# Optimization experiments

Hardware: AMD Instinct MI355X
Metric: run time of the kernel (lower is better)

Reference implementation:

```python
import jax, jax.numpy as jnp
import numpy as np

B, N, C = 8, 4096, 64          # graphs, points per graph, feature dim
RATIO = 0.25
M = int(N * RATIO)             # 1024 sampled centroids per graph
R = 0.2                        # radius (points live in the unit cube)
K = 64                         # max_num_neighbors in the forward
BIG = 1e10


def fps_single(pos):
    """Farthest point sampling on one cloud. pos: [N,3] -> [M] local indices.
    Deterministic start at index 0 (PyG uses a random start; math is identical)."""
    n = pos.shape[0]

    def step(carry, _):
        mind, last = carry
        d = jnp.sum((pos - pos[last]) ** 2, axis=-1)      # [N]
        mind = jnp.minimum(mind, d)
        nxt = jnp.argmax(mind)
        return (mind, nxt), nxt

    init = (jnp.full((n,), BIG, pos.dtype), jnp.int32(0))
    _, rest = jax.lax.scan(step, init, None, length=M - 1)
    return jnp.concatenate([jnp.zeros((1,), rest.dtype), rest])


def setup_inputs() -> dict:
    key = jax.random.key(0)
    ks = jax.random.split(key, 8)
    x = jax.random.normal(ks[0], (B * N, C), dtype=jnp.float32)
    pos = jax.random.uniform(ks[1], (B * N, 3), dtype=jnp.float32)
    batch = jnp.repeat(jnp.arange(B, dtype=jnp.int64), N)
    seed_idx = jnp.arange(B * N, dtype=jnp.int64)
    d_in, h, f_out = C + 3, 128, 256
    W1 = jax.random.normal(ks[2], (d_in, h), dtype=jnp.float32) / np.sqrt(d_in)
    b1 = jnp.zeros((h,), jnp.float32)
    W2 = jax.random.normal(ks[3], (h, h), dtype=jnp.float32) / np.sqrt(h)
    b2 = jnp.zeros((h,), jnp.float32)
    W3 = jax.random.normal(ks[4], (h, f_out), dtype=jnp.float32) / np.sqrt(h)
    b3 = jnp.zeros((f_out,), jnp.float32)
    return {"x": x, "pos": pos, "batch": batch, "seed_idx": seed_idx,
            "W1": W1, "b1": b1, "W2": W2, "b2": b2, "W3": W3, "b3": b3}


def reference(x, pos, batch, seed_idx, W1, b1, W2, b2, W3, b3):
    posb = pos.reshape(B, N, 3)
    xb = x.reshape(B, N, C)

    # --- FPS per graph (batch is block-contiguous with N points per graph) ---
    idx_local = jax.vmap(fps_single)(posb)                     # [B, M]
    ctr = jax.vmap(lambda p, i: p[i])(posb, idx_local)         # [B, M, 3]

    # --- radius neighbor search: up to K neighbors within r of each centroid ---
    d2 = jnp.sum((ctr[:, :, None, :] - posb[:, None, :, :]) ** 2, axis=-1)  # [B,M,N]
    d2m = jnp.where(d2 < R * R, d2, BIG)
    neg_d, nbr = jax.lax.top_k(-d2m, K)                        # K nearest within r
    valid = (-neg_d) < R * R                                   # [B, M, K]

    # --- PointConv: msg = MLP([x_j, pos_j - pos_i]), max-aggregate ---
    x_j = jax.vmap(lambda a, i: a[i])(xb, nbr)                 # [B, M, K, C]
    pos_j = jax.vmap(lambda p, i: p[i])(posb, nbr)             # [B, M, K, 3]
    msg = jnp.concatenate([x_j, pos_j - ctr[:, :, None, :]], axis=-1)  # [B,M,K,C+3]
    h = jax.nn.relu(msg @ W1 + b1)
    h = jax.nn.relu(h @ W2 + b2)
    h = jax.nn.relu(h @ W3 + b3)                               # [B, M, K, 256]
    h = jnp.where(valid[..., None], h, -BIG)
    out = jnp.max(h, axis=2)                                   # [B, M, 256]
    out = jnp.where(jnp.any(valid, axis=-1)[..., None], out, 0.0)

    # --- gather sampled outputs back to the flat layout ---
    idx_flat = (idx_local + jnp.arange(B)[:, None] * N).reshape(-1)  # [B*M]
    x_out = out.reshape(B * M, -1)
    pos_out = pos[idx_flat]
    batch_out = batch[idx_flat]
    seed_out = seed_idx[idx_flat]
    return x_out, pos_out, batch_out, seed_out
```

## Files before the change

### kernel.cpp

```cpp
#include <hip/hip_runtime.h>
#include <stdint.h>

#define BB 8
#define NN 4096
#define CC 64
#define MM 1024
#define EE (BB*MM)
#define KK 64
#define F3 256
#define SM 104
#define SH 136
#define CAP 768

typedef __bf16 bf16x8 __attribute__((ext_vector_type(8)));
typedef float floatx4 __attribute__((ext_vector_type(4)));

#define DPP_MAXSTEP(ctrl, rmask) { \
    unsigned o = (unsigned)__builtin_amdgcn_update_dpp(0, (int)v, ctrl, rmask, 0xf, false); \
    v = v > o ? v : o; }
__device__ __forceinline__ unsigned wave_umax_u32(unsigned v) {
  DPP_MAXSTEP(0x111, 0xf)
  DPP_MAXSTEP(0x112, 0xf)
  DPP_MAXSTEP(0x114, 0xf)
  DPP_MAXSTEP(0x118, 0xf)
  DPP_MAXSTEP(0x142, 0xa)
  DPP_MAXSTEP(0x143, 0xc)
  return (unsigned)__builtin_amdgcn_readlane((int)v, 63);
}
#define DPP_MINSTEP(ctrl, rmask) { \
    unsigned o = (unsigned)__builtin_amdgcn_update_dpp((int)0xffffffffu, (int)v, ctrl, rmask, 0xf, false); \
    v = v < o ? v : o; }
__device__ __forceinline__ unsigned wave_umin_u32(unsigned v) {
  DPP_MINSTEP(0x111, 0xf)
  DPP_MINSTEP(0x112, 0xf)
  DPP_MINSTEP(0x114, 0xf)
  DPP_MINSTEP(0x118, 0xf)
  DPP_MINSTEP(0x142, 0xa)
  DPP_MINSTEP(0x143, 0xc)
  return (unsigned)__builtin_amdgcn_readlane((int)v, 63);
}

__global__ __launch_bounds__(256) void fps_prep_kernel(
    const float* __restrict__ pos,
    const float* __restrict__ W1, const float* __restrict__ W2, const float* __restrict__ W3,
    int* __restrict__ fpsIdx, float* __restrict__ ctr,
    __bf16* __restrict__ W1t, __bf16* __restrict__ W2t, __bf16* __restrict__ W3t,
    float4* __restrict__ pos4) {
  __shared__ float4 sP4[NN];
  __shared__ unsigned long long sRed[2][4];
  const int blk = blockIdx.x;
  const int t = threadIdx.x;

  if (blk >= BB) {
    if (blk < 248) {
      const int i0 = (blk - 8) * 256 + t;
      if (i0 < 128 * 96) {
        const int n = i0 / 96, k = i0 % 96;
        W1t[i0] = (k < 67) ? (__bf16)W1[k * 128 + n] : (__bf16)0.0f;
      } else if (i0 < 128 * 96 + 128 * 128) {
        const int i = i0 - 128 * 96;
        const int n = i / 128, k = i % 128;
        W2t[i] = (__bf16)W2[k * 128 + n];
      } else {
        const int i = i0 - (128 * 96 + 128 * 128);
        const int n = i / 128, k = i % 128;
        W3t[i] = (__bf16)W3[k * 256 + n];
      }
    } else {
      const int i = (blk - 248) * 256 + t;
      pos4[i] = make_float4(pos[(long)i * 3 + 0], pos[(long)i * 3 + 1],
                            pos[(long)i * 3 + 2], 0.0f);
    }
    return;
  }

  const int g = blk;
  const int lane = t & 63, wv = t >> 6;
  float px[16], py[16], pz[16], mind[16];
#pragma unroll
  for (int j = 0; j < 16; ++j) {
    const int p = t + (j << 8);
    const long base = ((long)g * NN + p) * 3;
    px[j] = pos[base + 0];
    py[j] = pos[base + 1];
    pz[j] = pos[base + 2];
    mind[j] = 1e10f;
    sP4[p] = make_float4(px[j], py[j], pz[j], 0.0f);
  }
  __syncthreads();
  float wx = sP4[0].x, wy = sP4[0].y, wz = sP4[0].z;
  int win0 = 0, win1 = 0, win2 = 0, win3 = 0;
  for (int s = 1; s < MM; ++s) {
    unsigned bb = 0u, bidx = (unsigned)t;
#pragma unroll
    for (int j = 0; j < 16; ++j) {
      const float dx = __fsub_rn(px[j], wx);
      const float dy = __fsub_rn(py[j], wy);
      const float dz = __fsub_rn(pz[j], wz);
      const float d2 = __fadd_rn(__fadd_rn(__fmul_rn(dx, dx), __fmul_rn(dy, dy)), __fmul_rn(dz, dz));
      mind[j] = fminf(mind[j], d2);
      const unsigned mb = __float_as_uint(mind[j]);
      if (mb > bb) { bb = mb; bidx = (unsigned)(t + (j << 8)); }
    }
    const unsigned maxv = wave_umax_u32(bb);
    const unsigned cand = (bb == maxv) ? bidx : 0xffffffffu;
    const unsigned widx_w = wave_umin_u32(cand);
    if (lane == 0)
      sRed[s & 1][wv] = ((unsigned long long)maxv << 32) | (unsigned long long)(~widx_w);
    __syncthreads();
    unsigned long long m = sRed[s & 1][0];
#pragma unroll
    for (int w = 1; w < 4; ++w) {
      const unsigned long long o = sRed[s & 1][w];
      m = o > m ? o : m;
    }
    const int widx = (int)(~(unsigned)m);
    const float4 wp = sP4[widx];
    wx = wp.x; wy = wp.y; wz = wp.z;
    win0 = (s == t)       ? widx : win0;
    win1 = (s == t + 256) ? widx : win1;
    win2 = (s == t + 512) ? widx : win2;
    win3 = (s == t + 768) ? widx : win3;
  }
  {
    const long e0 = (long)g * MM + t;
    const float4 p0 = sP4[win0];
    fpsIdx[e0] = win0;
    ctr[e0 * 3 + 0] = p0.x; ctr[e0 * 3 + 1] = p0.y; ctr[e0 * 3 + 2] = p0.z;
    const long e1 = e0 + 256;
    const float4 p1 = sP4[win1];
    fpsIdx[e1] = win1;
    ctr[e1 * 3 + 0] = p1.x; ctr[e1 * 3 + 1] = p1.y; ctr[e1 * 3 + 2] = p1.z;
    const long e2 = e0 + 512;
    const float4 p2 = sP4[win2];
    fpsIdx[e2] = win2;
    ctr[e2 * 3 + 0] = p2.x; ctr[e2 * 3 + 1] = p2.y; ctr[e2 * 3 + 2] = p2.z;
    const long e3 = e0 + 768;
    const float4 p3 = sP4[win3];
    fpsIdx[e3] = win3;
    ctr[e3 * 3 + 0] = p3.x; ctr[e3 * 3 + 1] = p3.y; ctr[e3 * 3 + 2] = p3.z;
  }
}

__global__ __launch_bounds__(512) void mlp_kernel(const float* __restrict__ x,
    const float4* __restrict__ pos4, const float* __restrict__ ctr,
    const int* __restrict__ fpsIdx,
    const __bf16* __restrict__ W1t, const __bf16* __restrict__ W2t,
    const __bf16* __restrict__ W3t,
    const float* __restrict__ b1, const float* __restrict__ b2,
    const float* __restrict__ b3,
    float* __restrict__ outX, float* __restrict__ outP,
    float* __restrict__ outB, float* __restrict__ outS) {
  __shared__ __align__(16) __bf16 sMsg[64 * SM];
  __shared__ __align__(16) __bf16 sH[64 * SH];
  __shared__ int sSel[KK];
  __shared__ int sCnt;
  unsigned long long* sDI = (unsigned long long*)sMsg;

  const int e = blockIdx.x;
  const int t = threadIdx.x;
  const int b = e >> 10;
  const int lane = t & 63, wv = t >> 6;

  if (t == 0) sCnt = 0;
  const float cx = ctr[(long)e * 3 + 0];
  const float cy = ctr[(long)e * 3 + 1];
  const float cz = ctr[(long)e * 3 + 2];
  if (t < 3) outP[(long)e * 3 + t] = ctr[(long)e * 3 + t];
  if (t == 3) { outB[e] = (float)b; outS[e] = (float)(b * NN + fpsIdx[e]); }
  const float R2 = (float)(0.2 * 0.2);
  __syncthreads();

#pragma unroll
  for (int q = 0; q < NN / 512; ++q) {
    const int p = t + q * 512;
    const float4 P = pos4[b * NN + p];
    const float dx = __fsub_rn(cx, P.x);
    const float dy = __fsub_rn(cy, P.y);
    const float dz = __fsub_rn(cz, P.z);
    const float d2 = __fadd_rn(__fadd_rn(__fmul_rn(dx, dx), __fmul_rn(dy, dy)), __fmul_rn(dz, dz));
    const bool v = d2 < R2;
    const unsigned long long mask = __ballot(v);
    int wbase = 0;
    if (lane == 0 && mask) wbase = atomicAdd(&sCnt, (int)__popcll(mask));
    wbase = __shfl(wbase, 0);
    if (v) {
      const int off = wbase + (int)__popcll(mask & ((1ull << lane) - 1ull));
      if (off < CAP)
        sDI[off] = ((unsigned long long)__float_as_uint(d2) << 32) | (unsigned)p;
    }
  }
  __syncthreads();
  int cnt = sCnt; cnt = cnt > CAP ? CAP : cnt;
  const int nsel = cnt < KK ? cnt : KK;

  for (int i = t; i < cnt; i += 512) {
    const unsigned long long my = sDI[i];
    int rank = 0;
#pragma unroll 8
    for (int j = 0; j < cnt; ++j) rank += (sDI[j] < my) ? 1 : 0;
    if (rank < KK) sSel[rank] = (int)(unsigned)(my & 0xffffffffu);
  }
  __syncthreads();
  cnt = nsel;

  {
    const int r = t >> 3, p = t & 7;
    float4 a = make_float4(0.f, 0.f, 0.f, 0.f), c4 = a;
    if (r < cnt) {
      const float* xr = x + (long)(b * NN + sSel[r]) * CC + p * 8;
      a  = *(const float4*)xr;
      c4 = *(const float4*)(xr + 4);
    }
    __bf16 o[8] = {(__bf16)a.x, (__bf16)a.y, (__bf16)a.z, (__bf16)a.w,
                   (__bf16)c4.x, (__bf16)c4.y, (__bf16)c4.z, (__bf16)c4.w};
    *(uint4*)&sMsg[r * SM + p * 8] = *(uint4*)o;
  }
  if (t < 64) {
    const int r = t;
    __bf16 d0 = (__bf16)0.0f, d1 = (__bf16)0.0f, d2v = (__bf16)0.0f;
    if (r < cnt) {
      const float4 P = pos4[b * NN + sSel[r]];
      d0  = (__bf16)__fsub_rn(P.x, cx);
      d1  = (__bf16)__fsub_rn(P.y, cy);
      d2v = (__bf16)__fsub_rn(P.z, cz);
    }
    sMsg[r * SM + 64] = d0;
    sMsg[r * SM + 65] = d1;
    sMsg[r * SM + 66] = d2v;
    for (int c = 67; c < SM; ++c) sMsg[r * SM + c] = (__bf16)0.0f;
  }
  __syncthreads();

  const int l15 = lane & 15, quad = lane >> 4;
  {
    floatx4 acc[4] = {};
    const __bf16* wrow = W1t + (wv * 16 + l15) * 96;
#pragma unroll
    for (int ks = 0; ks < 3; ++ks) {
      const bf16x8 bfrag = *(const bf16x8*)(wrow + ks * 32 + quad * 8);
#pragma unroll
      for (int mt = 0; mt < 4; ++mt) {
        const bf16x8 afrag = *(const bf16x8*)&sMsg[(mt * 16 + l15) * SM + ks * 32 + quad * 8];
        acc[mt] = __builtin_amdgcn_mfma_f32_16x16x32_bf16(afrag, bfrag, acc[mt], 0, 0, 0);
      }
    }
    const int col = wv * 16 + l15;
    const float bias = b1[col];
#pragma unroll
    for (int mt = 0; mt < 4; ++mt)
#pragma unroll
      for (int rg = 0; rg < 4; ++rg) {
        const int row = mt * 16 + quad * 4 + rg;
        float v = acc[mt][rg] + bias;
        v = v > 0.0f ? v : 0.0f;
        sH[row * SH + col] = (__bf16)v;
      }
  }
  __syncthreads();
  {
    floatx4 acc[4] = {};
    const __bf16* wrow = W2t + (wv * 16 + l15) * 128;
#pragma unroll
    for (int ks = 0; ks < 4; ++ks) {
      const bf16x8 bfrag = *(const bf16x8*)(wrow + ks * 32 + quad * 8);
#pragma unroll
      for (int mt = 0; mt < 4; ++mt) {
        const bf16x8 afrag = *(const bf16x8*)&sH[(mt * 16 + l15) * SH + ks * 32 + quad * 8];
        acc[mt] = __builtin_amdgcn_mfma_f32_16x16x32_bf16(afrag, bfrag, acc[mt], 0, 0, 0);
      }
    }
    __syncthreads();
    const int col = wv * 16 + l15;
    const float bias = b2[col];
#pragma unroll
    for (int mt = 0; mt < 4; ++mt)
#pragma unroll
      for (int rg = 0; rg < 4; ++rg) {
        const int row = mt * 16 + quad * 4 + rg;
        float v = acc[mt][rg] + bias;
        v = v > 0.0f ? v : 0.0f;
        sH[row * SH + col] = (__bf16)v;
      }
  }
  __syncthreads();
  {
    floatx4 acc[2][4] = {};
#pragma unroll
    for (int ks = 0; ks < 4; ++ks) {
      bf16x8 afrag[4];
#pragma unroll
      for (int mt = 0; mt < 4; ++mt)
        afrag[mt] = *(const bf16x8*)&sH[(mt * 16 + l15) * SH + ks * 32 + quad * 8];
#pragma unroll
      for (int i = 0; i < 2; ++i) {
        const bf16x8 bfrag = *(const bf16x8*)(W3t + ((wv * 2 + i) * 16 + l15) * 128 + ks * 32 + quad * 8);
#pragma unroll
        for (int mt = 0; mt < 4; ++mt)
          acc[i][mt] = __builtin_amdgcn_mfma_f32_16x16x32_bf16(afrag[mt], bfrag, acc[i][mt], 0, 0, 0);
      }
    }
#pragma unroll
    for (int i = 0; i < 2; ++i) {
      const int col = (wv * 2 + i) * 16 + l15;
      const float bias = b3[col];
      float mx = 0.0f;
#pragma unroll
      for (int mt = 0; mt < 4; ++mt)
#pragma unroll
        for (int rg = 0; rg < 4; ++rg) {
          const int row = mt * 16 + quad * 4 + rg;
          float v = acc[i][mt][rg] + bias;
          v = v > 0.0f ? v : 0.0f;
          if (row < cnt) mx = fmaxf(mx, v);
        }
      mx = fmaxf(mx, __shfl_xor(mx, 16));
      mx = fmaxf(mx, __shfl_xor(mx, 32));
      if (quad == 0) outX[(long)e * F3 + col] = mx;
    }
  }
}

extern "C" void kernel_launch(void* const* d_in, const int* in_sizes, int n_in,
                              void* d_out, int out_size, void* d_ws, size_t ws_size,
                              hipStream_t stream) {
  const float* x   = (const float*)d_in[0];
  const float* pos = (const float*)d_in[1];
  const float* W1  = (const float*)d_in[4];
  const float* b1  = (const float*)d_in[5];
  const float* W2  = (const float*)d_in[6];
  const float* b2  = (const float*)d_in[7];
  const float* W3  = (const float*)d_in[8];
  const float* b3  = (const float*)d_in[9];

  char* ws = (char*)d_ws;
  int*    fpsIdx = (int*)(ws);
  float*  ctr    = (float*)(ws + 32768);
  __bf16* W1t    = (__bf16*)(ws + 131072);
  __bf16* W2t    = (__bf16*)(ws + 155648);
  __bf16* W3t    = (__bf16*)(ws + 188416);
  float4* pos4   = (float4*)(ws + 253952);

  float* outX = (float*)d_out;
  float* outP = outX + (long)EE * F3;
  float* outB = outP + (long)EE * 3;
  float* outS = outB + EE;

  fps_prep_kernel<<<376, 256, 0, stream>>>(pos, W1, W2, W3,
                                           fpsIdx, ctr, W1t, W2t, W3t, pos4);
  mlp_kernel<<<EE, 512, 0, stream>>>(x, pos4, ctr, fpsIdx, W1t, W2t, W3t,
                                     b1, b2, b3, outX, outP, outB, outS);
}
```

Baseline: 828.0 us.

## Fuse FPS and MLP into one persistent-ticket kernel with streaming progress flags

Merges the FPS/prep kernel and the per-centroid MLP kernel into one launch. Blocks take roles from an atomic ticket counter: the first eight run FPS and publish progress flags every 32 centroids, and the rest spin-wait on those flags so they can process centroids while FPS is still running. Centroid items are interleaved across graphs so the earliest ready centroids of all graphs are consumed first. The goal is to hide the serial FPS latency behind the MLP work. In exchange it adds spin-waiting, a memset launch, 64KB of shared memory per block that can lower occupancy, and it depends on the FPS blocks staying resident and running at raised priority.

```diff
diff --git a/kernel.cpp b/kernel.cpp
--- a/kernel.cpp
+++ b/kernel.cpp
@@ -40,283 +40,298 @@
   return (unsigned)__builtin_amdgcn_readlane((int)v, 63);
 }
 
-__global__ __launch_bounds__(256) void fps_prep_kernel(
-    const float* __restrict__ pos,
-    const float* __restrict__ W1, const float* __restrict__ W2, const float* __restrict__ W3,
+
+__global__ __launch_bounds__(512) void fused_kernel(
+    const float* __restrict__ x, const float* __restrict__ pos,
+    const float* __restrict__ W1, const float* __restrict__ b1,
+    const float* __restrict__ W2, const float* __restrict__ b2,
+    const float* __restrict__ W3, const float* __restrict__ b3,
     int* __restrict__ fpsIdx, float* __restrict__ ctr,
     __bf16* __restrict__ W1t, __bf16* __restrict__ W2t, __bf16* __restrict__ W3t,
-    float4* __restrict__ pos4) {
-  __shared__ float4 sP4[NN];
-  __shared__ unsigned long long sRed[2][4];
-  const int blk = blockIdx.x;
+    float4* __restrict__ pos4, unsigned* __restrict__ ctl,
+    float* __restrict__ outX, float* __restrict__ outP,
+    float* __restrict__ outB, float* __restrict__ outS) {
+  __shared__ __align__(16) unsigned char sBuf[65600];
+  __shared__ unsigned sRole;
+
   const int t = threadIdx.x;
 
-  if (blk >= BB) {
-    if (blk < 248) {
-      const int i0 = (blk - 8) * 256 + t;
-      if (i0 < 128 * 96) {
-        const int n = i0 / 96, k = i0 % 96;
-        W1t[i0] = (k < 67) ? (__bf16)W1[k * 128 + n] : (__bf16)0.0f;
-      } else if (i0 < 128 * 96 + 128 * 128) {
-        const int i = i0 - 128 * 96;
-        const int n = i / 128, k = i % 128;
-        W2t[i] = (__bf16)W2[k * 128 + n];
+  if (t == 0)
+    sRole = __hip_atomic_fetch_add(&ctl[288], 1u, __ATOMIC_RELAXED, __HIP_MEMORY_SCOPE_AGENT);
+  __syncthreads();
+  const unsigned role = sRole;
+
+  if (role < BB) {
+    const int g = (int)role;
+    float4* sP4 = (float4*)sBuf;
+    unsigned long long* sRed = (unsigned long long*)(sBuf + 65536);
+
+    for (int k = g * 11776 + t; k < (g + 1) * 11776; k += 512) {
+      if (k < 12288) {
+        const int n = k / 96, kk = k % 96;
+        W1t[k] = (kk < 67) ? (__bf16)W1[kk * 128 + n] : (__bf16)0.0f;
+      } else if (k < 28672) {
+        const int i = k - 12288, n = i / 128, kk = i % 128;
+        W2t[i] = (__bf16)W2[kk * 128 + n];
+      } else if (k < 61440) {
+        const int i = k - 28672, n = i / 128, kk = i % 128;
+        W3t[i] = (__bf16)W3[kk * 256 + n];
       } else {
-        const int i = i0 - (128 * 96 + 128 * 128);
-        const int n = i / 128, k = i % 128;
-        W3t[i] = (__bf16)W3[k * 256 + n];
-      }
-    } else {
-      const int i = (blk - 248) * 256 + t;
-      pos4[i] = make_float4(pos[(long)i * 3 + 0], pos[(long)i * 3 + 1],
-                            pos[(long)i * 3 + 2], 0.0f);
+        const int i = k - 61440;
+        pos4[i] = make_float4(pos[(long)i * 3 + 0], pos[(long)i * 3 + 1],
+                              pos[(long)i * 3 + 2], 0.0f);
+      }
+    }
+    __threadfence();
+    __syncthreads();
+    if (t == 0)
+      __hip_atomic_fetch_add(&ctl[0], 1u, __ATOMIC_RELEASE, __HIP_MEMORY_SCOPE_AGENT);
+
+    __builtin_amdgcn_s_setprio(1);
+
+    const int lane = t & 63, wv = t >> 6;
+    float px[16], py[16], pz[16], mind[16];
+    if (t < 256) {
+#pragma unroll
+      for (int j = 0; j < 16; ++j) {
+        const int p = t + (j << 8);
+        const long base = ((long)g * NN + p) * 3;
+        px[j] = pos[base + 0];
+        py[j] = pos[base + 1];
+        pz[j] = pos[base + 2];
+        mind[j] = 1e10f;
+        sP4[p] = make_float4(px[j], py[j], pz[j], 0.0f);
+      }
+    }
+    __syncthreads();
+    float wx = 0.f, wy = 0.f, wz = 0.f;
+    if (t < 256) { const float4 w0 = sP4[0]; wx = w0.x; wy = w0.y; wz = w0.z; }
+    if (t == 0) {
+      const long e0 = (long)g * MM;
+      ctr[e0 * 3 + 0] = px[0]; ctr[e0 * 3 + 1] = py[0]; ctr[e0 * 3 + 2] = pz[0];
+      fpsIdx[e0] = 0;
+    }
+    for (int s = 1; s < MM; ++s) {
+      if (t < 256) {
+        unsigned bb = 0u, bidx = (unsigned)t;
+#pragma unroll
+        for (int j = 0; j < 16; ++j) {
+          const float dx = __fsub_rn(px[j], wx);
+          const float dy = __fsub_rn(py[j], wy);
+          const float dz = __fsub_rn(pz[j], wz);
+          const float d2 = __fadd_rn(__fadd_rn(__fmul_rn(dx, dx), __fmul_rn(dy, dy)), __fmul_rn(dz, dz));
+          mind[j] = fminf(mind[j], d2);
+          const unsigned mb = __float_as_uint(mind[j]);
+          if (mb > bb) { bb = mb; bidx = (unsigned)(t + (j << 8)); }
+        }
+        const unsigned maxv = wave_umax_u32(bb);
+        const unsigned cand = (bb == maxv) ? bidx : 0xffffffffu;
+        const unsigned widx_w = wave_umin_u32(cand);
+        if (lane == 0)
+          sRed[(s & 1) * 4 + wv] = ((unsigned long long)maxv << 32) | (unsigned long long)(~widx_w);
+      }
+      __syncthreads();
+      if (t < 256) {
+        unsigned long long m = sRed[(s & 1) * 4 + 0];
+#pragma unroll
+        for (int w = 1; w < 4; ++w) {
+          const unsigned long long o = sRed[(s & 1) * 4 + w];
+          m = o > m ? o : m;
+        }
+        const int widx = (int)(~(unsigned)m);
+        const float4 wp = sP4[widx];
+        wx = wp.x; wy = wp.y; wz = wp.z;
+        if (t == 0) {
+          const long eo = (long)g * MM + s;
+          ctr[eo * 3 + 0] = wp.x; ctr[eo * 3 + 1] = wp.y; ctr[eo * 3 + 2] = wp.z;
+          fpsIdx[eo] = widx;
+          if ((s & 31) == 31)
+            __hip_atomic_store(&ctl[32 * (g + 1)], (unsigned)(s + 1),
+                               __ATOMIC_RELEASE, __HIP_MEMORY_SCOPE_AGENT);
+        }
+      }
     }
     return;
   }
 
-  const int g = blk;
-  const int lane = t & 63, wv = t >> 6;
-  float px[16], py[16], pz[16], mind[16];
-#pragma unroll
-  for (int j = 0; j < 16; ++j) {
-    const int p = t + (j << 8);
-    const long base = ((long)g * NN + p) * 3;
-    px[j] = pos[base + 0];
-    py[j] = pos[base + 1];
-    pz[j] = pos[base + 2];
-    mind[j] = 1e10f;
-    sP4[p] = make_float4(px[j], py[j], pz[j], 0.0f);
-  }
-  __syncthreads();
-  float wx = sP4[0].x, wy = sP4[0].y, wz = sP4[0].z;
-  int win0 = 0, win1 = 0, win2 = 0, win3 = 0;
-  for (int s = 1; s < MM; ++s) {
-    unsigned bb = 0u, bidx = (unsigned)t;
-#pragma unroll
-    for (int j = 0; j < 16; ++j) {
-      const float dx = __fsub_rn(px[j], wx);
-      const float dy = __fsub_rn(py[j], wy);
-      const float dz = __fsub_rn(pz[j], wz);
+  {
+    const int item = (int)role - BB;
+    if (item >= EE) return;
+    const int g = item & 7, sidx = item >> 3;
+    const int e = g * MM + sidx;
+    const int b = g;
+
+    __bf16* sMsg = (__bf16*)sBuf;
+    __bf16* sH   = (__bf16*)(sBuf + 13312);
+    int* sSel    = (int*)(sBuf + 30720);
+    int* sCnt    = (int*)(sBuf + 30976);
+    unsigned long long* sDI = (unsigned long long*)sBuf;
+
+    if (t == 0) {
+      while (__hip_atomic_load(&ctl[0], __ATOMIC_ACQUIRE, __HIP_MEMORY_SCOPE_AGENT) < (unsigned)BB)
+        __builtin_amdgcn_s_sleep(8);
+      while (__hip_atomic_load(&ctl[32 * (g + 1)], __ATOMIC_ACQUIRE, __HIP_MEMORY_SCOPE_AGENT)
+             <= (unsigned)sidx)
+        __builtin_amdgcn_s_sleep(8);
+      *sCnt = 0;
+    }
+    __syncthreads();
+
+    const int lane = t & 63, wv = t >> 6;
+    const float cx = ctr[(long)e * 3 + 0];
+    const float cy = ctr[(long)e * 3 + 1];
+    const float cz = ctr[(long)e * 3 + 2];
+    if (t < 3) outP[(long)e * 3 + t] = ctr[(long)e * 3 + t];
+    if (t == 3) { outB[e] = (float)b; outS[e] = (float)(b * NN + fpsIdx[e]); }
+    const float R2 = (float)(0.2 * 0.2);
+
+#pragma unroll
+    for (int q = 0; q < NN / 512; ++q) {
+      const int p = t + q * 512;
+      const float4 P = pos4[b * NN + p];
+      const float dx = __fsub_rn(cx, P.x);
+      const float dy = __fsub_rn(cy, P.y);
+      const float dz = __fsub_rn(cz, P.z);
       const float d2 = __fadd_rn(__fadd_rn(__fmul_rn(dx, dx), __fmul_rn(dy, dy)), __fmul_rn(dz, dz));
-      mind[j] = fminf(mind[j], d2);
-      const unsigned mb = __float_as_uint(mind[j]);
-      if (mb > bb) { bb = mb; bidx = (unsigned)(t + (j << 8)); }
-    }
-    const unsigned maxv = wave_umax_u32(bb);
-    const unsigned cand = (bb == maxv) ? bidx : 0xffffffffu;
-    const unsigned widx_w = wave_umin_u32(cand);
-    if (lane == 0)
-      sRed[s & 1][wv] = ((unsigned long long)maxv << 32) | (unsigned long long)(~widx_w);
-    __syncthreads();
-    unsigned long long m = sRed[s & 1][0];
-#pragma unroll
-    for (int w = 1; w < 4; ++w) {
-      const unsigned long long o = sRed[s & 1][w];
-      m = o > m ? o : m;
-    }
-    const int widx = (int)(~(unsigned)m);
-    const float4 wp = sP4[widx];
-    wx = wp.x; wy = wp.y; wz = wp.z;
-    win0 = (s == t)       ? widx : win0;
-    win1 = (s == t + 256) ? widx : win1;
-    win2 = (s == t + 512) ? widx : win2;
-    win3 = (s == t + 768) ? widx : win3;
-  }
-  {
-    const long e0 = (long)g * MM + t;
-    const float4 p0 = sP4[win0];
-    fpsIdx[e0] = win0;
-    ctr[e0 * 3 + 0] = p0.x; ctr[e0 * 3 + 1] = p0.y; ctr[e0 * 3 + 2] = p0.z;
-    const long e1 = e0 + 256;
-    const float4 p1 = sP4[win1];
-    fpsIdx[e1] = win1;
-    ctr[e1 * 3 + 0] = p1.x; ctr[e1 * 3 + 1] = p1.y; ctr[e1 * 3 + 2] = p1.z;
-    const long e2 = e0 + 512;
-    const float4 p2 = sP4[win2];
-    fpsIdx[e2] = win2;
-    ctr[e2 * 3 + 0] = p2.x; ctr[e2 * 3 + 1] = p2.y; ctr[e2 * 3 + 2] = p2.z;
-    const long e3 = e0 + 768;
-    const float4 p3 = sP4[win3];
-    fpsIdx[e3] = win3;
-    ctr[e3 * 3 + 0] = p3.x; ctr[e3 * 3 + 1] = p3.y; ctr[e3 * 3 + 2] = p3.z;
-  }
-}
-
-__global__ __launch_bounds__(512) void mlp_kernel(const float* __restrict__ x,
-    const float4* __restrict__ pos4, const float* __restrict__ ctr,
-    const int* __restrict__ fpsIdx,
-    const __bf16* __restrict__ W1t, const __bf16* __restrict__ W2t,
-    const __bf16* __restrict__ W3t,
-    const float* __restrict__ b1, const float* __restrict__ b2,
-    const float* __restrict__ b3,
-    float* __restrict__ outX, float* __restrict__ outP,
-    float* __restrict__ outB, float* __restrict__ outS) {
-  __shared__ __align__(16) __bf16 sMsg[64 * SM];
-  __shared__ __align__(16) __bf16 sH[64 * SH];
-  __shared__ int sSel[KK];
-  __shared__ int sCnt;
-  unsigned long long* sDI = (unsigned long long*)sMsg;
-
-  const int e = blockIdx.x;
-  const int t = threadIdx.x;
-  const int b = e >> 10;
-  const int lane = t & 63, wv = t >> 6;
-
-  if (t == 0) sCnt = 0;
-  const float cx = ctr[(long)e * 3 + 0];
-  const float cy = ctr[(long)e * 3 + 1];
-  const float cz = ctr[(long)e * 3 + 2];
-  if (t < 3) outP[(long)e * 3 + t] = ctr[(long)e * 3 + t];
-  if (t == 3) { outB[e] = (float)b; outS[e] = (float)(b * NN + fpsIdx[e]); }
-  const float R2 = (float)(0.2 * 0.2);
-  __syncthreads();
-
-#pragma unroll
-  for (int q = 0; q < NN / 512; ++q) {
-    const int p = t + q * 512;
-    const float4 P = pos4[b * NN + p];
-    const float dx = __fsub_rn(cx, P.x);
-    const float dy = __fsub_rn(cy, P.y);
-    const float dz = __fsub_rn(cz, P.z);
-    const float d2 = __fadd_rn(__fadd_rn(__fmul_rn(dx, dx), __fmul_rn(dy, dy)), __fmul_rn(dz, dz));
-    const bool v = d2 < R2;
-    const unsigned long long mask = __ballot(v);
-    int wbase = 0;
-    if (lane == 0 && mask) wbase = atomicAdd(&sCnt, (int)__popcll(mask));
-    wbase = __shfl(wbase, 0);
-    if (v) {
-      const int off = wbase + (int)__popcll(mask & ((1ull << lane) - 1ull));
-      if (off < CAP)
-        sDI[off] = ((unsigned long long)__float_as_uint(d2) << 32) | (unsigned)p;
-    }
-  }
-  __syncthreads();
-  int cnt = sCnt; cnt = cnt > CAP ? CAP : cnt;
-  const int nsel = cnt < KK ? cnt : KK;
-
-  for (int i = t; i < cnt; i += 512) {
-    const unsigned long long my = sDI[i];
-    int rank = 0;
+      const bool v = d2 < R2;
+      const unsigned long long mask = __ballot(v);
+      int wbase = 0;
+      if (lane == 0 && mask) wbase = atomicAdd(sCnt, (int)__popcll(mask));
+      wbase = __shfl(wbase, 0);
+      if (v) {
+        const int off = wbase + (int)__popcll(mask & ((1ull << lane) - 1ull));
+        if (off < CAP)
+          sDI[off] = ((unsigned long long)__float_as_uint(d2) << 32) | (unsigned)p;
+      }
+    }
+    __syncthreads();
+    int cnt = *sCnt; cnt = cnt > CAP ? CAP : cnt;
+    const int nsel = cnt < KK ? cnt : KK;
+
+    for (int i = t; i < cnt; i += 512) {
+      const unsigned long long my = sDI[i];
+      int rank = 0;
 #pragma unroll 8
-    for (int j = 0; j < cnt; ++j) rank += (sDI[j] < my) ? 1 : 0;
-    if (rank < KK) sSel[rank] = (int)(unsigned)(my & 0xffffffffu);
-  }
-  __syncthreads();
-  cnt = nsel;
-
-  {
-    const int r = t >> 3, p = t & 7;
-    float4 a = make_float4(0.f, 0.f, 0.f, 0.f), c4 = a;
-    if (r < cnt) {
-      const float* xr = x + (long)(b * NN + sSel[r]) * CC + p * 8;
-      a  = *(const float4*)xr;
-      c4 = *(const float4*)(xr + 4);
-    }
-    __bf16 o[8] = {(__bf16)a.x, (__bf16)a.y, (__bf16)a.z, (__bf16)a.w,
-                   (__bf16)c4.x, (__bf16)c4.y, (__bf16)c4.z, (__bf16)c4.w};
-    *(uint4*)&sMsg[r * SM + p * 8] = *(uint4*)o;
-  }
-  if (t < 64) {
-    const int r = t;
-    __bf16 d0 = (__bf16)0.0f, d1 = (__bf16)0.0f, d2v = (__bf16)0.0f;
-    if (r < cnt) {
-      const float4 P = pos4[b * NN + sSel[r]];
-      d0  = (__bf16)__fsub_rn(P.x, cx);
-      d1  = (__bf16)__fsub_rn(P.y, cy);
-      d2v = (__bf16)__fsub_rn(P.z, cz);
-    }
-    sMsg[r * SM + 64] = d0;
-    sMsg[r * SM + 65] = d1;
-    sMsg[r * SM + 66] = d2v;
-    for (int c = 67; c < SM; ++c) sMsg[r * SM + c] = (__bf16)0.0f;
-  }
-  __syncthreads();
-
-  const int l15 = lane & 15, quad = lane >> 4;
-  {
-    floatx4 acc[4] = {};
-    const __bf16* wrow = W1t + (wv * 16 + l15) * 96;
-#pragma unroll
-    for (int ks = 0; ks < 3; ++ks) {
-      const bf16x8 bfrag = *(const bf16x8*)(wrow + ks * 32 + quad * 8);
-#pragma unroll
-      for (int mt = 0; mt < 4; ++mt) {
-        const bf16x8 afrag = *(const bf16x8*)&sMsg[(mt * 16 + l15) * SM + ks * 32 + quad * 8];
-        acc[mt] = __builtin_amdgcn_mfma_f32_16x16x32_bf16(afrag, bfrag, acc[mt], 0, 0, 0);
-      }
-    }
-    const int col = wv * 16 + l15;
-    const float bias = b1[col];
-#pragma unroll
-    for (int mt = 0; mt < 4; ++mt)
-#pragma unroll
-      for (int rg = 0; rg < 4; ++rg) {
-        const int row = mt * 16 + quad * 4 + rg;
-        float v = acc[mt][rg] + bias;
-        v = v > 0.0f ? v : 0.0f;
-        sH[row * SH + col] = (__bf16)v;
-      }
-  }
-  __syncthreads();
-  {
-    floatx4 acc[4] = {};
-    const __bf16* wrow = W2t + (wv * 16 + l15) * 128;
-#pragma unroll
-    for (int ks = 0; ks < 4; ++ks) {
-      const bf16x8 bfrag = *(const bf16x8*)(wrow + ks * 32 + quad * 8);
-#pragma unroll
-      for (int mt = 0; mt < 4; ++mt) {
-        const bf16x8 afrag = *(const bf16x8*)&sH[(mt * 16 + l15) * SH + ks * 32 + quad * 8];
-        acc[mt] = __builtin_amdgcn_mfma_f32_16x16x32_bf16(afrag, bfrag, acc[mt], 0, 0, 0);
-      }
-    }
-    __syncthreads();
-    const int col = wv * 16 + l15;
-    const float bias = b2[col];
-#pragma unroll
-    for (int mt = 0; mt < 4; ++mt)
-#pragma unroll
-      for (int rg = 0; rg < 4; ++rg) {
-        const int row = mt * 16 + quad * 4 + rg;
-        float v = acc[mt][rg] + bias;
-        v = v > 0.0f ? v : 0.0f;
-        sH[row * SH + col] = (__bf16)v;
-      }
-  }
-  __syncthreads();
-  {
-    floatx4 acc[2][4] = {};
-#pragma unroll
-    for (int ks = 0; ks < 4; ++ks) {
-      bf16x8 afrag[4];
-#pragma unroll
-      for (int mt = 0; mt < 4; ++mt)
-        afrag[mt] = *(const bf16x8*)&sH[(mt * 16 + l15) * SH + ks * 32 + quad * 8];
-#pragma unroll
-      for (int i = 0; i < 2; ++i) {
-        const bf16x8 bfrag = *(const bf16x8*)(W3t + ((wv * 2 + i) * 16 + l15) * 128 + ks * 32 + quad * 8);
-#pragma unroll
-        for (int mt = 0; mt < 4; ++mt)
-          acc[i][mt] = __builtin_amdgcn_mfma_f32_16x16x32_bf16(afrag[mt], bfrag, acc[i][mt], 0, 0, 0);
-      }
-    }
-#pragma unroll
-    for (int i = 0; i < 2; ++i) {
-      const int col = (wv * 2 + i) * 16 + l15;
-      const float bias = b3[col];
-      float mx = 0.0f;
+      for (int j = 0; j < cnt; ++j) rank += (sDI[j] < my) ? 1 : 0;
+      if (rank < KK) sSel[rank] = (int)(unsigned)(my & 0xffffffffu);
+    }
+    __syncthreads();
+    cnt = nsel;
+
+    {
+      const int r = t >> 3, p = t & 7;
+      float4 a = make_float4(0.f, 0.f, 0.f, 0.f), c4 = a;
+      if (r < cnt) {
+        const float* xr = x + (long)(b * NN + sSel[r]) * CC + p * 8;
+        a  = *(const float4*)xr;
+        c4 = *(const float4*)(xr + 4);
+      }
+      __bf16 o[8] = {(__bf16)a.x, (__bf16)a.y, (__bf16)a.z, (__bf16)a.w,
+                     (__bf16)c4.x, (__bf16)c4.y, (__bf16)c4.z, (__bf16)c4.w};
+      *(uint4*)&sMsg[r * SM + p * 8] = *(uint4*)o;
+    }
+    if (t < 64) {
+      const int r = t;
+      __bf16 d0 = (__bf16)0.0f, d1 = (__bf16)0.0f, d2v = (__bf16)0.0f;
+      if (r < cnt) {
+        const float4 P = pos4[b * NN + sSel[r]];
+        d0  = (__bf16)__fsub_rn(P.x, cx);
+        d1  = (__bf16)__fsub_rn(P.y, cy);
+        d2v = (__bf16)__fsub_rn(P.z, cz);
+      }
+      sMsg[r * SM + 64] = d0;
+      sMsg[r * SM + 65] = d1;
+      sMsg[r * SM + 66] = d2v;
+      for (int c = 67; c < SM; ++c) sMsg[r * SM + c] = (__bf16)0.0f;
+    }
+    __syncthreads();
+
+    const int l15 = lane & 15, quad = lane >> 4;
+    {
+      floatx4 acc[4] = {};
+      const __bf16* wrow = W1t + (wv * 16 + l15) * 96;
+#pragma unroll
+      for (int ks = 0; ks < 3; ++ks) {
+        const bf16x8 bfrag = *(const bf16x8*)(wrow + ks * 32 + quad * 8);
+#pragma unroll
+        for (int mt = 0; mt < 4; ++mt) {
+          const bf16x8 afrag = *(const bf16x8*)&sMsg[(mt * 16 + l15) * SM + ks * 32 + quad * 8];
+          acc[mt] = __builtin_amdgcn_mfma_f32_16x16x32_bf16(afrag, bfrag, acc[mt], 0, 0, 0);
+        }
+      }
+      const int col = wv * 16 + l15;
+      const float bias = b1[col];
 #pragma unroll
       for (int mt = 0; mt < 4; ++mt)
 #pragma unroll
         for (int rg = 0; rg < 4; ++rg) {
           const int row = mt * 16 + quad * 4 + rg;
-          float v = acc[i][mt][rg] + bias;
+          float v = acc[mt][rg] + bias;
           v = v > 0.0f ? v : 0.0f;
-          if (row < cnt) mx = fmaxf(mx, v);
-        }
-      mx = fmaxf(mx, __shfl_xor(mx, 16));
-      mx = fmaxf(mx, __shfl_xor(mx, 32));
-      if (quad == 0) outX[(long)e * F3 + col] = mx;
+          sH[row * SH + col] = (__bf16)v;
+        }
+    }
+    __syncthreads();
+    {
+      floatx4 acc[4] = {};
+      const __bf16* wrow = W2t + (wv * 16 + l15) * 128;
+#pragma unroll
+      for (int ks = 0; ks < 4; ++ks) {
+        const bf16x8 bfrag = *(const bf16x8*)(wrow + ks * 32 + quad * 8);
+#pragma unroll
+        for (int mt = 0; mt < 4; ++mt) {
+          const bf16x8 afrag = *(const bf16x8*)&sH[(mt * 16 + l15) * SH + ks * 32 + quad * 8];
+          acc[mt] = __builtin_amdgcn_mfma_f32_16x16x32_bf16(afrag, bfrag, acc[mt], 0, 0, 0);
+        }
+      }
+      __syncthreads();
+      const int col = wv * 16 + l15;
+      const float bias = b2[col];
+#pragma unroll
+      for (int mt = 0; mt < 4; ++mt)
+#pragma unroll
+        for (int rg = 0; rg < 4; ++rg) {
+          const int row = mt * 16 + quad * 4 + rg;
+          float v = acc[mt][rg] + bias;
+          v = v > 0.0f ? v : 0.0f;
+          sH[row * SH + col] = (__bf16)v;
+        }
+    }
+    __syncthreads();
+    {
+      floatx4 acc[2][4] = {};
+#pragma unroll
+      for (int ks = 0; ks < 4; ++ks) {
+        bf16x8 afrag[4];
+#pragma unroll
+        for (int mt = 0; mt < 4; ++mt)
+          afrag[mt] = *(const bf16x8*)&sH[(mt * 16 + l15) * SH + ks * 32 + quad * 8];
+#pragma unroll
+        for (int i = 0; i < 2; ++i) {
+          const bf16x8 bfrag = *(const bf16x8*)(W3t + ((wv * 2 + i) * 16 + l15) * 128 + ks * 32 + quad * 8);
+#pragma unroll
+          for (int mt = 0; mt < 4; ++mt)
+            acc[i][mt] = __builtin_amdgcn_mfma_f32_16x16x32_bf16(afrag[mt], bfrag, acc[i][mt], 0, 0, 0);
+        }
+      }
+#pragma unroll
+      for (int i = 0; i < 2; ++i) {
+        const int col = (wv * 2 + i) * 16 + l15;
+        const float bias = b3[col];
+        float mx = 0.0f;
+#pragma unroll
+        for (int mt = 0; mt < 4; ++mt)
+#pragma unroll
+          for (int rg = 0; rg < 4; ++rg) {
+            const int row = mt * 16 + quad * 4 + rg;
+            float v = acc[i][mt][rg] + bias;
+            v = v > 0.0f ? v : 0.0f;
+            if (row < cnt) mx = fmaxf(mx, v);
+          }
+        mx = fmaxf(mx, __shfl_xor(mx, 16));
+        mx = fmaxf(mx, __shfl_xor(mx, 32));
+        if (quad == 0) outX[(long)e * F3 + col] = mx;
+      }
     }
   }
 }
@@ -340,14 +355,15 @@
   __bf16* W2t    = (__bf16*)(ws + 155648);
   __bf16* W3t    = (__bf16*)(ws + 188416);
   float4* pos4   = (float4*)(ws + 253952);
+  unsigned* ctl  = (unsigned*)(ws + 778240);
 
   float* outX = (float*)d_out;
   float* outP = outX + (long)EE * F3;
   float* outB = outP + (long)EE * 3;
   float* outS = outB + EE;
 
-  fps_prep_kernel<<<376, 256, 0, stream>>>(pos, W1, W2, W3,
-                                           fpsIdx, ctr, W1t, W2t, W3t, pos4);
-  mlp_kernel<<<EE, 512, 0, stream>>>(x, pos4, ctr, fpsIdx, W1t, W2t, W3t,
-                                     b1, b2, b3, outX, outP, outB, outS);
+  hipMemsetAsync(ctl, 0, 1280, stream);
+  fused_kernel<<<BB + EE, 512, 0, stream>>>(x, pos, W1, b1, W2, b2, W3, b3,
+                                            fpsIdx, ctr, W1t, W2t, W3t, pos4, ctl,
+                                            outX, outP, outB, outS);
 }
```

After: 904.8 us. 1.09x slower.

## Halve MLP block to 256 threads and alias shared buffers for occupancy

Applied to the files above, without the earlier changes.

The per-centroid MLP kernel now runs with 256 threads instead of 512. Each wave computes twice as many output column tiles, and loops cover the radius scan, gather and layer-3 passes. The message, hidden and candidate buffers now share one aliased shared-memory region, with extra barriers before hidden writes overwrite the message buffer. The goal is to cut LDS and register footprint so more blocks fit per CU, at the cost of more serial work per wave.

```diff
diff --git a/kernel.cpp b/kernel.cpp
--- a/kernel.cpp
+++ b/kernel.cpp
@@ -88,7 +88,8 @@
     sP4[p] = make_float4(px[j], py[j], pz[j], 0.0f);
   }
   __syncthreads();
-  float wx = sP4[0].x, wy = sP4[0].y, wz = sP4[0].z;
+  float wx, wy, wz;
+  { const float4 w0 = sP4[0]; wx = w0.x; wy = w0.y; wz = w0.z; }
   int win0 = 0, win1 = 0, win2 = 0, win3 = 0;
   for (int s = 1; s < MM; ++s) {
     unsigned bb = 0u, bidx = (unsigned)t;
@@ -142,7 +143,7 @@
   }
 }
 
-__global__ __launch_bounds__(512) void mlp_kernel(const float* __restrict__ x,
+__global__ __launch_bounds__(256, 6) void mlp_kernel(const float* __restrict__ x,
     const float4* __restrict__ pos4, const float* __restrict__ ctr,
     const int* __restrict__ fpsIdx,
     const __bf16* __restrict__ W1t, const __bf16* __restrict__ W2t,
@@ -151,18 +152,19 @@
     const float* __restrict__ b3,
     float* __restrict__ outX, float* __restrict__ outP,
     float* __restrict__ outB, float* __restrict__ outS) {
-  __shared__ __align__(16) __bf16 sMsg[64 * SM];
-  __shared__ __align__(16) __bf16 sH[64 * SH];
-  __shared__ int sSel[KK];
-  __shared__ int sCnt;
-  unsigned long long* sDI = (unsigned long long*)sMsg;
+  __shared__ __align__(16) unsigned char sBuf[17408 + 256 + 16];
+  __bf16* sMsg = (__bf16*)sBuf;
+  __bf16* sH   = (__bf16*)sBuf;
+  int* sSel    = (int*)(sBuf + 17408);
+  int* sCnt    = (int*)(sBuf + 17664);
+  unsigned long long* sDI = (unsigned long long*)sBuf;
 
   const int e = blockIdx.x;
   const int t = threadIdx.x;
   const int b = e >> 10;
   const int lane = t & 63, wv = t >> 6;
 
-  if (t == 0) sCnt = 0;
+  if (t == 0) *sCnt = 0;
   const float cx = ctr[(long)e * 3 + 0];
   const float cy = ctr[(long)e * 3 + 1];
   const float cz = ctr[(long)e * 3 + 2];
@@ -172,8 +174,8 @@
   __syncthreads();
 
 #pragma unroll
-  for (int q = 0; q < NN / 512; ++q) {
-    const int p = t + q * 512;
+  for (int q = 0; q < NN / 256; ++q) {
+    const int p = t + q * 256;
     const float4 P = pos4[b * NN + p];
     const float dx = __fsub_rn(cx, P.x);
     const float dy = __fsub_rn(cy, P.y);
@@ -182,7 +184,7 @@
     const bool v = d2 < R2;
     const unsigned long long mask = __ballot(v);
     int wbase = 0;
-    if (lane == 0 && mask) wbase = atomicAdd(&sCnt, (int)__popcll(mask));
+    if (lane == 0 && mask) wbase = atomicAdd(sCnt, (int)__popcll(mask));
     wbase = __shfl(wbase, 0);
     if (v) {
       const int off = wbase + (int)__popcll(mask & ((1ull << lane) - 1ull));
@@ -191,10 +193,10 @@
     }
   }
   __syncthreads();
-  int cnt = sCnt; cnt = cnt > CAP ? CAP : cnt;
+  int cnt = *sCnt; cnt = cnt > CAP ? CAP : cnt;
   const int nsel = cnt < KK ? cnt : KK;
 
-  for (int i = t; i < cnt; i += 512) {
+  for (int i = t; i < cnt; i += 256) {
     const unsigned long long my = sDI[i];
     int rank = 0;
 #pragma unroll 8
@@ -204,8 +206,9 @@
   __syncthreads();
   cnt = nsel;
 
-  {
-    const int r = t >> 3, p = t & 7;
+#pragma unroll
+  for (int pass = 0; pass < 2; ++pass) {
+    const int r = (t >> 3) + (pass << 5), p = t & 7;
     float4 a = make_float4(0.f, 0.f, 0.f, 0.f), c4 = a;
     if (r < cnt) {
       const float* xr = x + (long)(b * NN + sSel[r]) * CC + p * 8;
@@ -234,75 +237,93 @@
 
   const int l15 = lane & 15, quad = lane >> 4;
   {
-    floatx4 acc[4] = {};
-    const __bf16* wrow = W1t + (wv * 16 + l15) * 96;
+    floatx4 acc[2][4] = {};
 #pragma unroll
     for (int ks = 0; ks < 3; ++ks) {
-      const bf16x8 bfrag = *(const bf16x8*)(wrow + ks * 32 + quad * 8);
-#pragma unroll
-      for (int mt = 0; mt < 4; ++mt) {
-        const bf16x8 afrag = *(const bf16x8*)&sMsg[(mt * 16 + l15) * SM + ks * 32 + quad * 8];
-        acc[mt] = __builtin_amdgcn_mfma_f32_16x16x32_bf16(afrag, bfrag, acc[mt], 0, 0, 0);
-      }
-    }
-    const int col = wv * 16 + l15;
-    const float bias = b1[col];
-#pragma unroll
-    for (int mt = 0; mt < 4; ++mt)
-#pragma unroll
-      for (int rg = 0; rg < 4; ++rg) {
-        const int row = mt * 16 + quad * 4 + rg;
-        float v = acc[mt][rg] + bias;
-        v = v > 0.0f ? v : 0.0f;
-        sH[row * SH + col] = (__bf16)v;
-      }
-  }
-  __syncthreads();
-  {
-    floatx4 acc[4] = {};
-    const __bf16* wrow = W2t + (wv * 16 + l15) * 128;
-#pragma unroll
-    for (int ks = 0; ks < 4; ++ks) {
-      const bf16x8 bfrag = *(const bf16x8*)(wrow + ks * 32 + quad * 8);
-#pragma unroll
-      for (int mt = 0; mt < 4; ++mt) {
-        const bf16x8 afrag = *(const bf16x8*)&sH[(mt * 16 + l15) * SH + ks * 32 + quad * 8];
-        acc[mt] = __builtin_amdgcn_mfma_f32_16x16x32_bf16(afrag, bfrag, acc[mt], 0, 0, 0);
-      }
-    }
-    __syncthreads();
-    const int col = wv * 16 + l15;
-    const float bias = b2[col];
-#pragma unroll
-    for (int mt = 0; mt < 4; ++mt)
-#pragma unroll
-      for (int rg = 0; rg < 4; ++rg) {
-        const int row = mt * 16 + quad * 4 + rg;
-        float v = acc[mt][rg] + bias;
-        v = v > 0.0f ? v : 0.0f;
-        sH[row * SH + col] = (__bf16)v;
-      }
-  }
-  __syncthreads();
-  {
-    floatx4 acc[2][4] = {};
-#pragma unroll
-    for (int ks = 0; ks < 4; ++ks) {
       bf16x8 afrag[4];
 #pragma unroll
       for (int mt = 0; mt < 4; ++mt)
-        afrag[mt] = *(const bf16x8*)&sH[(mt * 16 + l15) * SH + ks * 32 + quad * 8];
+        afrag[mt] = *(const bf16x8*)&sMsg[(mt * 16 + l15) * SM + ks * 32 + quad * 8];
 #pragma unroll
       for (int i = 0; i < 2; ++i) {
-        const bf16x8 bfrag = *(const bf16x8*)(W3t + ((wv * 2 + i) * 16 + l15) * 128 + ks * 32 + quad * 8);
+        const bf16x8 bfrag = *(const bf16x8*)(W1t + ((wv * 2 + i) * 16 + l15) * 96 + ks * 32 + quad * 8);
 #pragma unroll
         for (int mt = 0; mt < 4; ++mt)
           acc[i][mt] = __builtin_amdgcn_mfma_f32_16x16x32_bf16(afrag[mt], bfrag, acc[i][mt], 0, 0, 0);
       }
     }
+    __syncthreads();
 #pragma unroll
     for (int i = 0; i < 2; ++i) {
       const int col = (wv * 2 + i) * 16 + l15;
+      const float bias = b1[col];
+#pragma unroll
+      for (int mt = 0; mt < 4; ++mt)
+#pragma unroll
+        for (int rg = 0; rg < 4; ++rg) {
+          const int row = mt * 16 + quad * 4 + rg;
+          float v = acc[i][mt][rg] + bias;
+          v = v > 0.0f ? v : 0.0f;
+          sH[row * SH + col] = (__bf16)v;
+        }
+    }
+  }
+  __syncthreads();
+  {
+    floatx4 acc[2][4] = {};
+#pragma unroll
+    for (int ks = 0; ks < 4; ++ks) {
+      bf16x8 afrag[4];
+#pragma unroll
+      for (int mt = 0; mt < 4; ++mt)
+        afrag[mt] = *(const bf16x8*)&sH[(mt * 16 + l15) * SH + ks * 32 + quad * 8];
+#pragma unroll
+      for (int i = 0; i < 2; ++i) {
+        const bf16x8 bfrag = *(const bf16x8*)(W2t + ((wv * 2 + i) * 16 + l15) * 128 + ks * 32 + quad * 8);
+#pragma unroll
+        for (int mt = 0; mt < 4; ++mt)
+          acc[i][mt] = __builtin_amdgcn_mfma_f32_16x16x32_bf16(afrag[mt], bfrag, acc[i][mt], 0, 0, 0);
+      }
+    }
+    __syncthreads();
+#pragma unroll
+    for (int i = 0; i < 2; ++i) {
+      const int col = (wv * 2 + i) * 16 + l15;
+      const float bias = b2[col];
+#pragma unroll
+      for (int mt = 0; mt < 4; ++mt)
+#pragma unroll
+        for (int rg = 0; rg < 4; ++rg) {
+          const int row = mt * 16 + quad * 4 + rg;
+          float v = acc[i][mt][rg] + bias;
+          v = v > 0.0f ? v : 0.0f;
+          sH[row * SH + col] = (__bf16)v;
+        }
+    }
+  }
+  __syncthreads();
+#pragma unroll
+  for (int pp = 0; pp < 2; ++pp) {
+    floatx4 acc[2][4] = {};
+#pragma unroll
+    for (int ks = 0; ks < 4; ++ks) {
+      bf16x8 afrag[4];
+#pragma unroll
+      for (int mt = 0; mt < 4; ++mt)
+        afrag[mt] = *(const bf16x8*)&sH[(mt * 16 + l15) * SH + ks * 32 + quad * 8];
+#pragma unroll
+      for (int i = 0; i < 2; ++i) {
+        const int nt = wv * 4 + pp * 2 + i;
+        const bf16x8 bfrag = *(const bf16x8*)(W3t + (nt * 16 + l15) * 128 + ks * 32 + quad * 8);
+#pragma unroll
+        for (int mt = 0; mt < 4; ++mt)
+          acc[i][mt] = __builtin_amdgcn_mfma_f32_16x16x32_bf16(afrag[mt], bfrag, acc[i][mt], 0, 0, 0);
+      }
+    }
+#pragma unroll
+    for (int i = 0; i < 2; ++i) {
+      const int nt = wv * 4 + pp * 2 + i;
+      const int col = nt * 16 + l15;
       const float bias = b3[col];
       float mx = 0.0f;
 #pragma unroll
@@ -348,6 +369,6 @@
 
   fps_prep_kernel<<<376, 256, 0, stream>>>(pos, W1, W2, W3,
                                            fpsIdx, ctr, W1t, W2t, W3t, pos4);
-  mlp_kernel<<<EE, 512, 0, stream>>>(x, pos4, ctr, fpsIdx, W1t, W2t, W3t,
+  mlp_kernel<<<EE, 256, 0, stream>>>(x, pos4, ctr, fpsIdx, W1t, W2t, W3t,
                                      b1, b2, b3, outX, outP, outB, outS);
 }
```

New measurement: 892.5 us. 1.08x slower.
